# Kernel tuning notes

Measured on AMD Instinct MI355X. Metric: run time of the kernel, lower is better.

## Reference

```python
import jax, jax.numpy as jnp
import numpy as np

EPS = 1e-12

def _l2norm(x):
    return x / jnp.maximum(jnp.linalg.norm(x, axis=-1, keepdims=True), EPS)

def setup_inputs() -> dict:
    key = jax.random.key(0)
    ks = jax.random.split(key, 11)
    B, L, HID, M = 64, 512, 768, 128
    R, P, T = 64, 8, 32
    return {
        "hidden_states": jax.random.normal(ks[0], (B, L, HID), dtype=jnp.float32),
        "ctx_mask": jax.random.randint(ks[1], (B, L), 0, 2, dtype=jnp.int32),
        "between_mask": jax.random.randint(ks[2], (B, L), 0, 2, dtype=jnp.int32),
        "subj_type_id": jax.random.randint(ks[3], (B,), 0, T, dtype=jnp.int32),
        "obj_type_id": jax.random.randint(ks[4], (B,), 0, T, dtype=jnp.int32),
        "subj_first": jax.random.randint(ks[5], (B,), 0, 2, dtype=jnp.int32),
        "proj_W": jax.random.normal(ks[6], (HID, M), dtype=jnp.float32) * 0.02,
        "label_probes": jax.random.normal(ks[7], (R, P, M), dtype=jnp.float32) * 0.02,
        "subj_type_W": jax.random.normal(ks[8], (T, M), dtype=jnp.float32) * 0.02,
        "obj_type_W": jax.random.normal(ks[9], (T, M), dtype=jnp.float32) * 0.02,
        "dir_W": jax.random.normal(ks[10], (2, M), dtype=jnp.float32) * 0.02,
    }

def reference(hidden_states, ctx_mask, between_mask, subj_type_id, obj_type_id,
              subj_first, proj_W, label_probes, subj_type_W, obj_type_W, dir_W):
    # Document token embeddings: project + L2 normalize. [B, L, M]
    D = _l2norm(hidden_states @ proj_W)

    between = between_mask.astype(bool)
    ctx = ctx_mask.astype(bool)
    has_between = jnp.any(between, axis=1)  # [B]
    evidence = jnp.where(has_between[:, None], between, ctx)  # [B, L]

    # Conditioned probes: [B, R, P, M]
    Q = (label_probes[None]
         + subj_type_W[subj_type_id][:, None, None]
         + obj_type_W[obj_type_id][:, None, None]
         + dir_W[subj_first][:, None, None])
    Q = _l2norm(Q)

    # MaxSim: [B, R, P, L]
    sim = jnp.einsum('brhm,blm->brhl', Q, D)
    sim = jnp.where(evidence[:, None, None, :], sim, -10000.0)
    mx = sim.max(axis=3)                        # [B, R, P]
    mx = jnp.where(mx > -1000.0, mx, 0.0)       # zero out fully-masked probes
    logits = mx.sum(axis=2)                     # [B, R]
    return logits
```

## Files before the change

kernel.cpp:

```cpp
#include <hip/hip_runtime.h>
#include <hip/hip_bf16.h>

typedef __attribute__((ext_vector_type(8))) __bf16 bf16x8;
typedef __attribute__((ext_vector_type(4))) float f32x4;

#define B_   64
#define L_   512
#define HID_ 768
#define M_   128
#define R_   64
#define P_   8

__device__ __forceinline__ int swz(int row, int k, int stride) {
    return row * stride + (k ^ ((row & 7) << 3));
}
__device__ __forceinline__ int swz4(int row, int k) {
    return row * 128 + (k ^ ((row & 15) << 3));
}

#define GLL16(gp, lp)                                                        \
    __builtin_amdgcn_global_load_lds(                                        \
        (const __attribute__((address_space(1))) void*)(gp),                 \
        (__attribute__((address_space(3))) void*)(lp), 16, 0, 0)

__device__ __forceinline__ bf16x8 cvt8(float4 f0, float4 f1) {
    bf16x8 v;
    v[0]=(__bf16)f0.x; v[1]=(__bf16)f0.y; v[2]=(__bf16)f0.z; v[3]=(__bf16)f0.w;
    v[4]=(__bf16)f1.x; v[5]=(__bf16)f1.y; v[6]=(__bf16)f1.z; v[7]=(__bf16)f1.w;
    return v;
}

__global__ __launch_bounds__(256) void k_wt(const float* __restrict__ W,
                                            __bf16* __restrict__ Wt) {
    int idx = blockIdx.x * 256 + threadIdx.x;
    int k = idx >> 7, n = idx & 127;
    int c = k >> 6, kk = k & 63;
    Wt[c * 8192 + n * 64 + (kk ^ ((n & 7) << 3))] = (__bf16)W[idx];
}

__global__ __launch_bounds__(512, 4) void k_proj(const float* __restrict__ hidden,
                                                 const __bf16* __restrict__ Wt,
                                                 __bf16* __restrict__ D) {
    __shared__ __align__(16) __bf16 Al[2][64 * 64];
    __shared__ __align__(16) __bf16 Bl[2][128 * 64];
    __shared__ float nbuf[2][64];
    const int t = threadIdx.x;
    const int lane = t & 63, w = t >> 6;
    const int rlo = lane & 15, g = lane >> 4;
    const int rb = w & 3, ch = w >> 2;
    const int row0 = blockIdx.x * 512 + blockIdx.y * 64;

    f32x4 acc[4] = {};

    const int ar = t >> 3;
    const int ac = (t & 7) * 8;
    const float* arow = hidden + (size_t)(row0 + ar) * HID_ + ac;

    GLL16(Wt + w * 1024 + lane * 8,       &Bl[0][w * 1024]);
    GLL16(Wt + w * 1024 + 512 + lane * 8, &Bl[0][w * 1024 + 512]);
    {
        float4 f0 = *(const float4*)(arow);
        float4 f1 = *(const float4*)(arow + 4);
        *(bf16x8*)&Al[0][swz(ar, ac, 64)] = cvt8(f0, f1);
    }
    __syncthreads();

    for (int ci = 0; ci < 12; ++ci) {
        const int cur = ci & 1;
        const bool pre = ci < 11;
        float4 f0, f1;
        if (pre) {
            const __bf16* wsrc = Wt + (ci + 1) * 8192 + w * 1024;
            GLL16(wsrc + lane * 8,       &Bl[cur ^ 1][w * 1024]);
            GLL16(wsrc + 512 + lane * 8, &Bl[cur ^ 1][w * 1024 + 512]);
            const float* src = arow + (ci + 1) * 64;
            f0 = *(const float4*)(src);
            f1 = *(const float4*)(src + 4);
        }
#pragma unroll
        for (int s = 0; s < 2; ++s) {
            int kk = s * 32 + g * 8;
            bf16x8 aF = *(const bf16x8*)&Al[cur][swz(rb * 16 + rlo, kk, 64)];
#pragma unroll
            for (int c = 0; c < 4; ++c) {
                bf16x8 bF = *(const bf16x8*)&Bl[cur][swz(ch * 64 + c * 16 + rlo, kk, 64)];
                acc[c] = __builtin_amdgcn_mfma_f32_16x16x32_bf16(aF, bF, acc[c], 0, 0, 0);
            }
        }
        if (pre) {
            *(bf16x8*)&Al[cur ^ 1][swz(ar, ac, 64)] = cvt8(f0, f1);
        }
        __syncthreads();
    }

    float ss[4] = {0.f, 0.f, 0.f, 0.f};
#pragma unroll
    for (int c = 0; c < 4; ++c)
#pragma unroll
        for (int r = 0; r < 4; ++r) ss[r] += acc[c][r] * acc[c][r];
#pragma unroll
    for (int r = 0; r < 4; ++r)
#pragma unroll
        for (int off = 1; off < 16; off <<= 1) ss[r] += __shfl_xor(ss[r], off);
    if (rlo == 0) {
#pragma unroll
        for (int r = 0; r < 4; ++r) nbuf[ch][rb * 16 + g * 4 + r] = ss[r];
    }
    __syncthreads();
    float sc[4];
#pragma unroll
    for (int r = 0; r < 4; ++r) {
        float tot = nbuf[0][rb * 16 + g * 4 + r] + nbuf[1][rb * 16 + g * 4 + r];
        sc[r] = 1.0f / fmaxf(sqrtf(tot), 1e-12f);
    }

    __bf16* Dst = (__bf16*)Al;
#pragma unroll
    for (int c = 0; c < 4; ++c)
#pragma unroll
        for (int r = 0; r < 4; ++r) {
            int row = rb * 16 + g * 4 + r;
            int col = ch * 64 + c * 16 + rlo;
            Dst[swz4(row, col)] = (__bf16)(acc[c][r] * sc[r]);
        }
    __syncthreads();
#pragma unroll
    for (int h = 0; h < 2; ++h) {
        int row = (t >> 4) + h * 32;
        int seg = t & 15;
        bf16x8 v = *(const bf16x8*)&Dst[row * 128 + seg * 8];
        *(bf16x8*)(D + (size_t)(row0 + row) * M_ + seg * 8) = v;
    }
}

__global__ __launch_bounds__(256) void k_sim(const float* __restrict__ lp,
                                             const float* __restrict__ sW,
                                             const float* __restrict__ oW,
                                             const float* __restrict__ dW,
                                             const int* __restrict__ st,
                                             const int* __restrict__ ot,
                                             const int* __restrict__ sf,
                                             const int* __restrict__ ctx,
                                             const int* __restrict__ btw,
                                             const __bf16* __restrict__ D,
                                             float* __restrict__ out) {
    __shared__ float evl[L_];
    __shared__ float pmx[4][64];
    __shared__ int anyf;
    const int t = threadIdx.x;
    const int lane = t & 63, w = t >> 6;
    const int rlo = lane & 15, g = lane >> 4;
    const int b = blockIdx.x, pt = blockIdx.y;

    if (t == 0) anyf = 0;
    __syncthreads();
    int v0 = btw[b * L_ + t], v1 = btw[b * L_ + t + 256];
    int c0 = ctx[b * L_ + t], c1 = ctx[b * L_ + t + 256];
    if (v0 | v1) anyf = 1;
    __syncthreads();
    const int any = anyf;
    evl[t]       = (any ? v0 : c0) ? 1.0f : 0.0f;
    evl[t + 256] = (any ? v1 : c1) ? 1.0f : 0.0f;

    const int sb = st[b], ob = ot[b], db = sf[b];
    const float* sv = sW + sb * M_;
    const float* ov = oW + ob * M_;
    const float* dv = dW + db * M_;
    bf16x8 qF[4][4];
#pragma unroll
    for (int pt2 = 0; pt2 < 4; ++pt2) {
        const float* lpp = lp + (size_t)(pt * 64 + pt2 * 16 + rlo) * M_;
        float qv[32];
        float ssq = 0.f;
#pragma unroll
        for (int ks = 0; ks < 4; ++ks) {
#pragma unroll
            for (int h = 0; h < 2; ++h) {
                const int m0 = ks * 32 + g * 8 + h * 4;
                float4 a  = *(const float4*)(lpp + m0);
                float4 s4 = *(const float4*)(sv + m0);
                float4 o4 = *(const float4*)(ov + m0);
                float4 d4 = *(const float4*)(dv + m0);
                float x0 = a.x + s4.x + o4.x + d4.x;
                float x1 = a.y + s4.y + o4.y + d4.y;
                float x2 = a.z + s4.z + o4.z + d4.z;
                float x3 = a.w + s4.w + o4.w + d4.w;
                qv[ks * 8 + h * 4 + 0] = x0;
                qv[ks * 8 + h * 4 + 1] = x1;
                qv[ks * 8 + h * 4 + 2] = x2;
                qv[ks * 8 + h * 4 + 3] = x3;
                ssq += x0 * x0 + x1 * x1 + x2 * x2 + x3 * x3;
            }
        }
        ssq += __shfl_xor(ssq, 16);
        ssq += __shfl_xor(ssq, 32);
        const float scq = 1.0f / fmaxf(sqrtf(ssq), 1e-12f);
#pragma unroll
        for (int ks = 0; ks < 4; ++ks)
#pragma unroll
            for (int j = 0; j < 8; ++j)
                qF[pt2][ks][j] = (__bf16)(qv[ks * 8 + j] * scq);
    }
    __syncthreads();

    const __bf16* Db = D + (size_t)b * L_ * M_;
    float vmax[4][4];
#pragma unroll
    for (int pt2 = 0; pt2 < 4; ++pt2)
#pragma unroll
        for (int r = 0; r < 4; ++r) vmax[pt2][r] = -1e30f;

#pragma unroll 2
    for (int i = 0; i < 8; ++i) {
        const int tt = w * 8 + i;
        const __bf16* rowp = Db + (size_t)(tt * 16 + rlo) * M_;
        f32x4 pacc[4] = {};
#pragma unroll
        for (int ks = 0; ks < 4; ++ks) {
            bf16x8 bF = *(const bf16x8*)(rowp + ((ks * 32 + g * 8) ^ (rlo << 3)));
            pacc[0] = __builtin_amdgcn_mfma_f32_16x16x32_bf16(qF[0][ks], bF, pacc[0], 0, 0, 0);
            pacc[1] = __builtin_amdgcn_mfma_f32_16x16x32_bf16(qF[1][ks], bF, pacc[1], 0, 0, 0);
            pacc[2] = __builtin_amdgcn_mfma_f32_16x16x32_bf16(qF[2][ks], bF, pacc[2], 0, 0, 0);
            pacc[3] = __builtin_amdgcn_mfma_f32_16x16x32_bf16(qF[3][ks], bF, pacc[3], 0, 0, 0);
        }
        const float e = evl[tt * 16 + rlo];
#pragma unroll
        for (int pt2 = 0; pt2 < 4; ++pt2)
#pragma unroll
            for (int r = 0; r < 4; ++r) {
                float sv2 = (e > 0.5f) ? pacc[pt2][r] : -1e4f;
                vmax[pt2][r] = fmaxf(vmax[pt2][r], sv2);
            }
    }

#pragma unroll
    for (int pt2 = 0; pt2 < 4; ++pt2)
#pragma unroll
        for (int r = 0; r < 4; ++r)
#pragma unroll
            for (int off = 1; off < 16; off <<= 1)
                vmax[pt2][r] = fmaxf(vmax[pt2][r], __shfl_xor(vmax[pt2][r], off));

    if (rlo == 0) {
#pragma unroll
        for (int pt2 = 0; pt2 < 4; ++pt2)
#pragma unroll
            for (int r = 0; r < 4; ++r)
                pmx[w][pt2 * 16 + g * 4 + r] = vmax[pt2][r];
    }
    __syncthreads();

    if (t < 64) {
        float m = fmaxf(fmaxf(pmx[0][t], pmx[1][t]), fmaxf(pmx[2][t], pmx[3][t]));
        m = (m > -1000.0f) ? m : 0.0f;
        m += __shfl_xor(m, 1);
        m += __shfl_xor(m, 2);
        m += __shfl_xor(m, 4);
        if ((t & 7) == 0) out[b * R_ + pt * 8 + (t >> 3)] = m;
    }
}

extern "C" void kernel_launch(void* const* d_in, const int* in_sizes, int n_in,
                              void* d_out, int out_size, void* d_ws, size_t ws_size,
                              hipStream_t stream) {
    const float* hidden = (const float*)d_in[0];
    const int*   ctx    = (const int*)d_in[1];
    const int*   btw    = (const int*)d_in[2];
    const int*   st     = (const int*)d_in[3];
    const int*   ot     = (const int*)d_in[4];
    const int*   sf     = (const int*)d_in[5];
    const float* W      = (const float*)d_in[6];
    const float* lp     = (const float*)d_in[7];
    const float* sW     = (const float*)d_in[8];
    const float* oW     = (const float*)d_in[9];
    const float* dW     = (const float*)d_in[10];
    float* out = (float*)d_out;

    char* ws = (char*)d_ws;
    __bf16* Wt = (__bf16*)ws;
    __bf16* D  = (__bf16*)(ws + 196608);

    k_wt  <<<(HID_ * M_) / 256, 256, 0, stream>>>(W, Wt);
    k_proj<<<dim3(B_, 8), 512, 0, stream>>>(hidden, Wt, D);
    k_sim <<<dim3(B_, 8), 256, 0, stream>>>(lp, sW, oW, dW, st, ot, sf, ctx, btw, D, out);
}
```

Before: 51.30 us.

## Fuse projection and MaxSim into one kernel with a cross-block max reduction

```diff
diff --git a/kernel.cpp b/kernel.cpp
--- a/kernel.cpp
+++ b/kernel.cpp
@@ -38,17 +38,29 @@
     Wt[c * 8192 + n * 64 + (kk ^ ((n & 7) << 3))] = (__bf16)W[idx];
 }
 
-__global__ __launch_bounds__(512, 4) void k_proj(const float* __restrict__ hidden,
-                                                 const __bf16* __restrict__ Wt,
-                                                 __bf16* __restrict__ D) {
+__global__ __launch_bounds__(512, 4) void k_projsim(
+        const float* __restrict__ hidden, const __bf16* __restrict__ Wt,
+        const float* __restrict__ lp, const float* __restrict__ sW,
+        const float* __restrict__ oW, const float* __restrict__ dW,
+        const int* __restrict__ st, const int* __restrict__ ot,
+        const int* __restrict__ sf, const int* __restrict__ ctx,
+        const int* __restrict__ btw, float* __restrict__ pm) {
     __shared__ __align__(16) __bf16 Al[2][64 * 64];
     __shared__ __align__(16) __bf16 Bl[2][128 * 64];
     __shared__ float nbuf[2][64];
+    __shared__ float evl[64];
+    __shared__ int anyf;
     const int t = threadIdx.x;
     const int lane = t & 63, w = t >> 6;
     const int rlo = lane & 15, g = lane >> 4;
     const int rb = w & 3, ch = w >> 2;
-    const int row0 = blockIdx.x * 512 + blockIdx.y * 64;
+    const int b = blockIdx.x, j = blockIdx.y;
+    const int row0 = b * L_ + j * 64;
+
+    if (t == 0) anyf = 0;
+    const int bt = btw[b * L_ + t];
+    int btww = 0, ctxw = 0;
+    if (t < 64) { btww = btw[row0 + t]; ctxw = ctx[row0 + t]; }
 
     f32x4 acc[4] = {};
 
@@ -64,6 +76,7 @@
         *(bf16x8*)&Al[0][swz(ar, ac, 64)] = cvt8(f0, f1);
     }
     __syncthreads();
+    if (bt) anyf = 1;
 
     for (int ci = 0; ci < 12; ++ci) {
         const int cur = ci & 1;
@@ -114,53 +127,18 @@
         sc[r] = 1.0f / fmaxf(sqrtf(tot), 1e-12f);
     }
 
-    __bf16* Dst = (__bf16*)Al;
+    __bf16* Dl = (__bf16*)Al;
 #pragma unroll
     for (int c = 0; c < 4; ++c)
 #pragma unroll
         for (int r = 0; r < 4; ++r) {
             int row = rb * 16 + g * 4 + r;
             int col = ch * 64 + c * 16 + rlo;
-            Dst[swz4(row, col)] = (__bf16)(acc[c][r] * sc[r]);
-        }
+            Dl[swz4(row, col)] = (__bf16)(acc[c][r] * sc[r]);
+        }
+    const int any = anyf;
+    if (t < 64) evl[t] = ((any ? btww : ctxw) != 0) ? 1.0f : 0.0f;
     __syncthreads();
-#pragma unroll
-    for (int h = 0; h < 2; ++h) {
-        int row = (t >> 4) + h * 32;
-        int seg = t & 15;
-        bf16x8 v = *(const bf16x8*)&Dst[row * 128 + seg * 8];
-        *(bf16x8*)(D + (size_t)(row0 + row) * M_ + seg * 8) = v;
-    }
-}
-
-__global__ __launch_bounds__(256) void k_sim(const float* __restrict__ lp,
-                                             const float* __restrict__ sW,
-                                             const float* __restrict__ oW,
-                                             const float* __restrict__ dW,
-                                             const int* __restrict__ st,
-                                             const int* __restrict__ ot,
-                                             const int* __restrict__ sf,
-                                             const int* __restrict__ ctx,
-                                             const int* __restrict__ btw,
-                                             const __bf16* __restrict__ D,
-                                             float* __restrict__ out) {
-    __shared__ float evl[L_];
-    __shared__ float pmx[4][64];
-    __shared__ int anyf;
-    const int t = threadIdx.x;
-    const int lane = t & 63, w = t >> 6;
-    const int rlo = lane & 15, g = lane >> 4;
-    const int b = blockIdx.x, pt = blockIdx.y;
-
-    if (t == 0) anyf = 0;
-    __syncthreads();
-    int v0 = btw[b * L_ + t], v1 = btw[b * L_ + t + 256];
-    int c0 = ctx[b * L_ + t], c1 = ctx[b * L_ + t + 256];
-    if (v0 | v1) anyf = 1;
-    __syncthreads();
-    const int any = anyf;
-    evl[t]       = (any ? v0 : c0) ? 1.0f : 0.0f;
-    evl[t + 256] = (any ? v1 : c1) ? 1.0f : 0.0f;
 
     const int sb = st[b], ob = ot[b], db = sf[b];
     const float* sv = sW + sb * M_;
@@ -169,7 +147,7 @@
     bf16x8 qF[4][4];
 #pragma unroll
     for (int pt2 = 0; pt2 < 4; ++pt2) {
-        const float* lpp = lp + (size_t)(pt * 64 + pt2 * 16 + rlo) * M_;
+        const float* lpp = lp + (size_t)(w * 64 + pt2 * 16 + rlo) * M_;
         float qv[32];
         float ssq = 0.f;
 #pragma unroll
@@ -198,26 +176,22 @@
 #pragma unroll
         for (int ks = 0; ks < 4; ++ks)
 #pragma unroll
-            for (int j = 0; j < 8; ++j)
-                qF[pt2][ks][j] = (__bf16)(qv[ks * 8 + j] * scq);
-    }
-    __syncthreads();
-
-    const __bf16* Db = D + (size_t)b * L_ * M_;
+            for (int qj = 0; qj < 8; ++qj)
+                qF[pt2][ks][qj] = (__bf16)(qv[ks * 8 + qj] * scq);
+    }
+
     float vmax[4][4];
 #pragma unroll
     for (int pt2 = 0; pt2 < 4; ++pt2)
 #pragma unroll
         for (int r = 0; r < 4; ++r) vmax[pt2][r] = -1e30f;
 
-#pragma unroll 2
-    for (int i = 0; i < 8; ++i) {
-        const int tt = w * 8 + i;
-        const __bf16* rowp = Db + (size_t)(tt * 16 + rlo) * M_;
+#pragma unroll
+    for (int tt = 0; tt < 4; ++tt) {
         f32x4 pacc[4] = {};
 #pragma unroll
         for (int ks = 0; ks < 4; ++ks) {
-            bf16x8 bF = *(const bf16x8*)(rowp + ((ks * 32 + g * 8) ^ (rlo << 3)));
+            bf16x8 bF = *(const bf16x8*)&Dl[swz4(tt * 16 + rlo, ks * 32 + g * 8)];
             pacc[0] = __builtin_amdgcn_mfma_f32_16x16x32_bf16(qF[0][ks], bF, pacc[0], 0, 0, 0);
             pacc[1] = __builtin_amdgcn_mfma_f32_16x16x32_bf16(qF[1][ks], bF, pacc[1], 0, 0, 0);
             pacc[2] = __builtin_amdgcn_mfma_f32_16x16x32_bf16(qF[2][ks], bF, pacc[2], 0, 0, 0);
@@ -242,22 +216,27 @@
                 vmax[pt2][r] = fmaxf(vmax[pt2][r], __shfl_xor(vmax[pt2][r], off));
 
     if (rlo == 0) {
+        float* dst = pm + ((size_t)b * 8 + j) * 512 + w * 64;
 #pragma unroll
         for (int pt2 = 0; pt2 < 4; ++pt2)
 #pragma unroll
             for (int r = 0; r < 4; ++r)
-                pmx[w][pt2 * 16 + g * 4 + r] = vmax[pt2][r];
-    }
-    __syncthreads();
-
-    if (t < 64) {
-        float m = fmaxf(fmaxf(pmx[0][t], pmx[1][t]), fmaxf(pmx[2][t], pmx[3][t]));
-        m = (m > -1000.0f) ? m : 0.0f;
-        m += __shfl_xor(m, 1);
-        m += __shfl_xor(m, 2);
-        m += __shfl_xor(m, 4);
-        if ((t & 7) == 0) out[b * R_ + pt * 8 + (t >> 3)] = m;
-    }
+                dst[pt2 * 16 + g * 4 + r] = vmax[pt2][r];
+    }
+}
+
+__global__ __launch_bounds__(512) void k_reduce(const float* __restrict__ pm,
+                                                float* __restrict__ out) {
+    const int b = blockIdx.x, t = threadIdx.x;
+    float m = -1e30f;
+#pragma unroll
+    for (int j = 0; j < 8; ++j)
+        m = fmaxf(m, pm[((size_t)b * 8 + j) * 512 + t]);
+    m = (m > -1000.0f) ? m : 0.0f;
+    m += __shfl_xor(m, 1);
+    m += __shfl_xor(m, 2);
+    m += __shfl_xor(m, 4);
+    if ((t & 7) == 0) out[b * R_ + (t >> 3)] = m;
 }
 
 extern "C" void kernel_launch(void* const* d_in, const int* in_sizes, int n_in,
@@ -278,9 +257,10 @@
 
     char* ws = (char*)d_ws;
     __bf16* Wt = (__bf16*)ws;
-    __bf16* D  = (__bf16*)(ws + 196608);
-
-    k_wt  <<<(HID_ * M_) / 256, 256, 0, stream>>>(W, Wt);
-    k_proj<<<dim3(B_, 8), 512, 0, stream>>>(hidden, Wt, D);
-    k_sim <<<dim3(B_, 8), 256, 0, stream>>>(lp, sW, oW, dW, st, ot, sf, ctx, btw, D, out);
-}
+    float*  pm = (float*)(ws + 196608);
+
+    k_wt     <<<(HID_ * M_) / 256, 256, 0, stream>>>(W, Wt);
+    k_projsim<<<dim3(B_, 8), 512, 0, stream>>>(hidden, Wt, lp, sW, oW, dW,
+                                               st, ot, sf, ctx, btw, pm);
+    k_reduce <<<B_, 512, 0, stream>>>(pm, out);
+}
```

New measurement: 74.89 us. 1.46x slower.
